# Kernel tuning notes

Hardware: AMD Instinct MI355X
Metric: run time of the kernel (lower is better)

## Reference

```python
import jax, jax.numpy as jnp
import numpy as np

NL_IN = 0.5      # init kwarg nl_in
CONS = 1e-10     # epsilon added to rates
POISSON_GAIN = 20.0

def setup_inputs() -> dict:
    key = jax.random.key(0)
    k1, k2 = jax.random.split(key)
    shape = (8, 4, 28, 256, 256)  # (bs, c, s, h, w)
    spec_data = jax.random.uniform(k1, shape, dtype=jnp.float32)
    filt = jax.random.uniform(k2, shape, dtype=jnp.float32)
    return {"spec_data": spec_data, "filter": filt}

def reference(spec_data, filter):
    # cap_data = sum over (channel, spectral) dims -> [bs, h, w], then [bs, h, w, 1]
    cap = jnp.sum(spec_data * filter, axis=(1, 2))[..., None]

    # noise synthesis (need_noise=True path)
    poisson_t = jnp.full_like(cap, POISSON_GAIN * NL_IN)
    dark_t = jnp.full_like(cap, 1.0 * NL_IN)
    gauss_t = jnp.full_like(cap, 1.0 * NL_IN)
    peak = cap + CONS

    key = jax.random.key(1)
    kp, kd, kg = jax.random.split(key, 3)
    pnoisy = jax.random.poisson(kp, peak).astype(cap.dtype)
    dnoisy = jax.random.poisson(kd, dark_t).astype(cap.dtype)
    gnoisy = jax.random.normal(kg, cap.shape, dtype=cap.dtype) * gauss_t

    noisy = (pnoisy + dnoisy + gnoisy) * poisson_t / 255.0
    return (noisy, peak, dark_t, gauss_t ** 2)
```

## Files before the change

kernel.cpp:

```cpp
#include <hip/hip_runtime.h>
#include <cstdint>
#include <cstddef>

#pragma clang fp contract(off)

#define N_PIX    524288
#define CSPLANES 112
#define PLANE    65536
#define DCH      48

struct TF2 { uint32_t a, b; };

__host__ __device__ constexpr uint32_t rotl32(uint32_t x, int d) {
  return (x << d) | (x >> (32 - d));
}

__host__ __device__ constexpr TF2 threefry(uint32_t k0, uint32_t k1,
                                           uint32_t c0, uint32_t c1) {
  uint32_t ks2 = k0 ^ k1 ^ 0x1BD11BDAu;
  uint32_t x0 = c0 + k0;
  uint32_t x1 = c1 + k1;
  const int R0[4] = {13, 15, 26, 6};
  const int R1[4] = {17, 29, 16, 24};
  for (int i = 0; i < 4; ++i) { x0 += x1; x1 = rotl32(x1, R0[i]); x1 ^= x0; }
  x0 += k1;  x1 += ks2 + 1u;
  for (int i = 0; i < 4; ++i) { x0 += x1; x1 = rotl32(x1, R1[i]); x1 ^= x0; }
  x0 += ks2; x1 += k0 + 2u;
  for (int i = 0; i < 4; ++i) { x0 += x1; x1 = rotl32(x1, R0[i]); x1 ^= x0; }
  x0 += k0;  x1 += k1 + 3u;
  for (int i = 0; i < 4; ++i) { x0 += x1; x1 = rotl32(x1, R1[i]); x1 ^= x0; }
  x0 += k1;  x1 += ks2 + 4u;
  for (int i = 0; i < 4; ++i) { x0 += x1; x1 = rotl32(x1, R0[i]); x1 ^= x0; }
  x0 += ks2; x1 += k0 + 5u;
  return TF2{x0, x1};
}

struct Chains {
  uint32_t kg0, kg1;
  uint32_t rj0a[DCH], rj0b[DCH], rj1a[DCH], rj1b[DCH];
  uint32_t kda[DCH], kdb[DCH];
  uint32_t kpa[DCH], kpb[DCH];
};

__host__ __device__ constexpr Chains make_chains() {
  Chains c{};
  TF2 kp = threefry(0u, 1u, 0u, 0u);
  TF2 kd = threefry(0u, 1u, 0u, 1u);
  TF2 kg = threefry(0u, 1u, 0u, 2u);
  c.kg0 = kg.a; c.kg1 = kg.b;
  {
    uint32_t a = kp.a, b = kp.b;
    for (int i = 0; i < DCH; ++i) {
      TF2 nk = threefry(a, b, 0u, 0u);
      TF2 s0 = threefry(a, b, 0u, 1u);
      TF2 s1 = threefry(a, b, 0u, 2u);
      c.rj0a[i] = s0.a; c.rj0b[i] = s0.b;
      c.rj1a[i] = s1.a; c.rj1b[i] = s1.b;
      a = nk.a; b = nk.b;
    }
  }
  {
    uint32_t a = kd.a, b = kd.b;
    for (int i = 0; i < DCH; ++i) {
      TF2 nk = threefry(a, b, 0u, 0u);
      TF2 sk = threefry(a, b, 0u, 1u);
      c.kda[i] = sk.a; c.kdb[i] = sk.b;
      a = nk.a; b = nk.b;
    }
  }
  {
    uint32_t a = kp.a, b = kp.b;
    for (int i = 0; i < DCH; ++i) {
      TF2 nk = threefry(a, b, 0u, 0u);
      TF2 sk = threefry(a, b, 0u, 1u);
      c.kpa[i] = sk.a; c.kpb[i] = sk.b;
      a = nk.a; b = nk.b;
    }
  }
  return c;
}

__constant__ Chains G = make_chains();

__device__ inline float u01(uint32_t k0, uint32_t k1, uint32_t j) {
  TF2 r = threefry(k0, k1, 0u, j);
  uint32_t bits = r.a ^ r.b;
  return __uint_as_float((bits >> 9) | 0x3F800000u) - 1.0f;
}

__device__ inline float xla_lgamma(float x_in) {
  float z = x_in - 1.0f;
  float x = 1.0f;
  x = x + 676.520368121885098567009190444019f    / ((z + 0.0f) + 1.0f);
  x = x + (-1259.13921672240287047156078755283f) / ((z + 1.0f) + 1.0f);
  x = x + 771.3234287776530788486528258894f      / ((z + 2.0f) + 1.0f);
  x = x + (-176.61502916214059906584551354f)     / ((z + 3.0f) + 1.0f);
  x = x + 12.507343278686904814458936853f        / ((z + 4.0f) + 1.0f);
  x = x + (-0.13857109526572011689554707f)       / ((z + 5.0f) + 1.0f);
  x = x + 9.984369578019570859563e-6f            / ((z + 6.0f) + 1.0f);
  x = x + 1.50563273514931155834e-7f             / ((z + 7.0f) + 1.0f);
  float t = 7.5f + z;
  float log_t = 2.0149030205422647f + log1pf(z / 7.5f);
  return 0.91893853320467274178f + ((z + 0.5f) - t / log_t) * log_t + logf(x);
}

__device__ inline float xla_erfinv(float xx) {
  float w = -log1pf(-(xx * xx));
  float p;
  if (w < 5.0f) {
    float ww = w - 2.5f;
    p = 2.81022636e-08f;
    p = 3.43273939e-07f + p * ww;
    p = -3.5233877e-06f + p * ww;
    p = -4.39150654e-06f + p * ww;
    p = 0.00021858087f + p * ww;
    p = -0.00125372503f + p * ww;
    p = -0.00417768164f + p * ww;
    p = 0.246640727f + p * ww;
    p = 1.50140941f + p * ww;
  } else {
    float ww = sqrtf(w) - 3.0f;
    p = -0.000200214257f;
    p = 0.000100950558f + p * ww;
    p = 0.00134934322f + p * ww;
    p = -0.00367342844f + p * ww;
    p = 0.00573950773f + p * ww;
    p = -0.0076224613f + p * ww;
    p = 0.00943887047f + p * ww;
    p = 1.00167406f + p * ww;
    p = 2.83297682f + p * ww;
  }
  return p * xx;
}

__device__ inline float xla_normal(uint32_t j) {
  const float lo = -0.999999940395355224609375f;
  float f = u01(G.kg0, G.kg1, j);
  float u = f * (1.0f - lo) + lo;
  u = fmaxf(lo, u);
  return 1.41421356237309504880f * xla_erfinv(u);
}

__device__ inline int knuth_sample(const uint32_t* ka, const uint32_t* kb,
                                   uint32_t j, float lam) {
  const float neg = -lam;
  int k = 0;
  float lp = 0.0f;
  #pragma unroll 1
  for (int i = 0; i < DCH; ++i) {
    if (!(lp > neg)) break;
    ++k;
    float uu = u01(ka[i], kb[i], j);
    lp = lp + logf(uu);
  }
  return k - 1;
}

struct RejC { float lam, loglam, a, b, inva, vr; };

__device__ inline RejC make_rc(float lam) {
  RejC rc;
  rc.lam = lam;
  rc.loglam = logf(lam);
  rc.b = 0.931f + 2.53f * sqrtf(lam);
  rc.a = -0.059f + 0.02483f * rc.b;
  rc.inva = 1.1239f + 1.1328f / (rc.b - 3.4f);
  rc.vr = 0.9277f - 3.6224f / (rc.b - 2.0f);
  return rc;
}

__device__ inline bool rej_step(const RejC& rc, uint32_t j, int i, float* kout) {
  float u = u01(G.rj0a[i], G.rj0b[i], j) - 0.5f;
  float v = u01(G.rj1a[i], G.rj1b[i], j);
  float us = 0.5f - fabsf(u);
  float k = floorf(((2.0f * rc.a / us + rc.b) * u + rc.lam) + 0.43f);
  *kout = k;
  bool accept1 = (us >= 0.07f) && (v <= rc.vr);
  if (accept1) return true;
  bool reject = (k < 0.0f) || ((us < 0.013f) && (v > us));
  if (reject) return false;
  float s = logf(v * rc.inva / (rc.a / (us * us) + rc.b));
  float t = (-rc.lam + k * rc.loglam) - xla_lgamma(k + 1.0f);
  return s <= t;
}

__device__ inline unsigned first_accept(const RejC& rc, uint32_t j) {
  unsigned F = DCH;
  #pragma unroll 1
  for (int i = 0; i < DCH; ++i) {
    float kc;
    if (rej_step(rc, j, i, &kc)) { F = (unsigned)(i + 1); break; }
  }
  return F;
}

__device__ inline float resolve_pix(const RejC& rc, float peak, uint32_t j, int T) {
  if (peak >= 10.0f) {
    float kk = -1.0f;
    #pragma unroll 1
    for (int i = T - 1; i >= 0; --i) {
      float kc;
      if (rej_step(rc, j, i, &kc)) { kk = kc; break; }
    }
    return (float)(int)kk;
  } else if (peak <= 0.0f) {
    return 0.0f;
  } else {
    return (float)knuth_sample(G.kpa, G.kpb, j, peak);
  }
}

__global__ __launch_bounds__(256) void reduce_kernel(const float* __restrict__ spec,
                                                     const float* __restrict__ filt,
                                                     float* __restrict__ out) {
  const int tid = threadIdx.x;
  const int pixbase = blockIdx.x << 10;
  const int b_img = pixbase >> 16;
  const int hw = (pixbase & 65535) + (tid << 2);
  const size_t base = (size_t)b_img * ((size_t)CSPLANES * PLANE) + (size_t)hw;
  const float* sp = spec + base;
  const float* fp = filt + base;

  float4 acc = make_float4(0.f, 0.f, 0.f, 0.f);
  #pragma unroll 1
  for (int c = 0; c < CSPLANES; c += 8) {
    float4 ss[8], ff[8];
    #pragma unroll
    for (int i = 0; i < 8; ++i) ss[i] = *reinterpret_cast<const float4*>(sp + (size_t)(c + i) * PLANE);
    #pragma unroll
    for (int i = 0; i < 8; ++i) ff[i] = *reinterpret_cast<const float4*>(fp + (size_t)(c + i) * PLANE);
    __builtin_amdgcn_sched_group_barrier(0x020, 16, 0);
    #pragma unroll
    for (int i = 0; i < 8; ++i) {
      acc.x = acc.x + ss[i].x * ff[i].x;
      acc.y = acc.y + ss[i].y * ff[i].y;
      acc.z = acc.z + ss[i].z * ff[i].z;
      acc.w = acc.w + ss[i].w * ff[i].w;
    }
    __builtin_amdgcn_sched_group_barrier(0x002, 64, 0);
  }

  const int j = pixbase + (tid << 2);
  float4 pk = make_float4(acc.x + 1e-10f, acc.y + 1e-10f,
                          acc.z + 1e-10f, acc.w + 1e-10f);
  *reinterpret_cast<float4*>(out + N_PIX + j) = pk;
}

__global__ __launch_bounds__(256) void fmax_kernel(const float* __restrict__ out,
                                                   unsigned* __restrict__ sync) {
  const int j = (blockIdx.x << 8) + threadIdx.x;
  const float pk = out[N_PIX + j];
  const RejC rc = make_rc(pk);
  unsigned F = first_accept(rc, (uint32_t)j);

  for (int off = 32; off; off >>= 1) {
    unsigned o = (unsigned)__shfl_down((int)F, off, 64);
    F = F > o ? F : o;
  }
  __shared__ unsigned sred[4];
  if ((threadIdx.x & 63) == 0) sred[threadIdx.x >> 6] = F;
  __syncthreads();
  if (threadIdx.x == 0) {
    unsigned m = sred[0];
    #pragma unroll
    for (int i = 1; i < 4; ++i) m = m > sred[i] ? m : sred[i];
    __hip_atomic_fetch_max(&sync[0], m, __ATOMIC_RELAXED, __HIP_MEMORY_SCOPE_AGENT);
  }
}

__global__ __launch_bounds__(256) void resolve_kernel(float* __restrict__ out,
                                                      const unsigned* __restrict__ sync) {
  const int j = (blockIdx.x << 8) + threadIdx.x;
  const int T = (int)__hip_atomic_load(&sync[0], __ATOMIC_RELAXED, __HIP_MEMORY_SCOPE_AGENT);
  const float pk = out[N_PIX + j];

  const float d = (float)knuth_sample(G.kda, G.kdb, (uint32_t)j, 0.5f);
  const float g = xla_normal((uint32_t)j) * 0.5f;
  const RejC rc = make_rc(pk);
  const float pv = resolve_pix(rc, pk, (uint32_t)j, T);
  const float n = ((pv + d) + g) * 10.0f / 255.0f;

  out[j]             = n;
  out[2 * N_PIX + j] = 0.5f;
  out[3 * N_PIX + j] = 0.25f;
}

extern "C" void kernel_launch(void* const* d_in, const int* in_sizes, int n_in,
                              void* d_out, int out_size, void* d_ws, size_t ws_size,
                              hipStream_t stream) {
  (void)in_sizes; (void)n_in; (void)out_size; (void)ws_size;
  const float* spec = (const float*)d_in[0];
  const float* filt = (const float*)d_in[1];
  float* out = (float*)d_out;
  unsigned* sync = (unsigned*)d_ws;
  (void)hipMemsetAsync(d_ws, 0, 2 * sizeof(unsigned), stream);
  hipLaunchKernelGGL(reduce_kernel, dim3(512), dim3(256), 0, stream, spec, filt, out);
  hipLaunchKernelGGL(fmax_kernel, dim3(2048), dim3(256), 0, stream, out, sync);
  hipLaunchKernelGGL(resolve_kernel, dim3(2048), dim3(256), 0, stream, out, sync);
}
```

Baseline: 502.6 us.

## Stream reduction through LDS with async loads and fuse fmax pass

Rewrites the channel-spectral reduction so each wave issues direct global-to-LDS loads into a double buffer, waits on vmcnt and consumes the previous stage while the next is in flight. The separate fmax kernel is folded into the reduction, so each thread computes first-accept indices for its four pixels and atomically max-reduces them without a re-read and an extra launch. The cost is 64KB of LDS per block, which limits occupancy. Per-thread work after the reduce also grows fourfold on only 512 blocks, less parallel than the old 2048-block fmax kernel.

Result: no change. 494.3 us (-1.7%).

```diff
diff --git a/kernel.cpp b/kernel.cpp
--- a/kernel.cpp
+++ b/kernel.cpp
@@ -210,10 +210,55 @@
   }
 }
 
-__global__ __launch_bounds__(256) void reduce_kernel(const float* __restrict__ spec,
-                                                     const float* __restrict__ filt,
-                                                     float* __restrict__ out) {
+typedef float f32x4 __attribute__((ext_vector_type(4)));
+
+__device__ __forceinline__ void glds16(const float* g, float* l) {
+  __builtin_amdgcn_global_load_lds(
+      (const __attribute__((address_space(1))) void*)g,
+      (__attribute__((address_space(3))) void*)l,
+      16 , 0 , 0 );
+}
+
+#define WAITC(N)                                                          \
+  asm volatile("s_waitcnt vmcnt(" #N ")" ::: "memory");                   \
+  __builtin_amdgcn_sched_barrier(0);
+
+#define LGKM0                                                             \
+  asm volatile("s_waitcnt lgkmcnt(0)" ::: "memory");                      \
+  __builtin_amdgcn_sched_barrier(0);
+
+#define STAGE(B, CBASE)                                                   \
+  {                                                                       \
+    _Pragma("unroll")                                                     \
+    for (int s = 0; s < 4; ++s)                                           \
+      glds16(sp + (size_t)((CBASE) + s) * PLANE,                          \
+             wbase + (B) * 2048 + s * 256);                               \
+    _Pragma("unroll")                                                     \
+    for (int s = 0; s < 4; ++s)                                           \
+      glds16(fp + (size_t)((CBASE) + s) * PLANE,                          \
+             wbase + (B) * 2048 + (4 + s) * 256);                         \
+  }
+
+#define CONSUME(B)                                                        \
+  {                                                                       \
+    _Pragma("unroll")                                                     \
+    for (int s = 0; s < 4; ++s) {                                         \
+      f32x4 sv = *reinterpret_cast<f32x4*>(wbase + (B) * 2048 + s * 256 + (lane << 2));       \
+      f32x4 fv = *reinterpret_cast<f32x4*>(wbase + (B) * 2048 + (4 + s) * 256 + (lane << 2)); \
+      ax = ax + sv[0] * fv[0];                                            \
+      ay = ay + sv[1] * fv[1];                                            \
+      az = az + sv[2] * fv[2];                                            \
+      aw = aw + sv[3] * fv[3];                                            \
+    }                                                                     \
+  }
+
+__global__ __launch_bounds__(256, 2) void reduce_kernel(const float* __restrict__ spec,
+                                                        const float* __restrict__ filt,
+                                                        float* __restrict__ out,
+                                                        unsigned* __restrict__ sync) {
   const int tid = threadIdx.x;
+  const int wid = tid >> 6;
+  const int lane = tid & 63;
   const int pixbase = blockIdx.x << 10;
   const int b_img = pixbase >> 16;
   const int hw = (pixbase & 65535) + (tid << 2);
@@ -221,46 +266,56 @@
   const float* sp = spec + base;
   const float* fp = filt + base;
 
-  float4 acc = make_float4(0.f, 0.f, 0.f, 0.f);
+  __shared__ float lds[16384];
+  float* wbase = &lds[wid << 12];
+
+  float ax = 0.f, ay = 0.f, az = 0.f, aw = 0.f;
+
+  STAGE(0, 0);
+  STAGE(1, 4);
   #pragma unroll 1
-  for (int c = 0; c < CSPLANES; c += 8) {
-    float4 ss[8], ff[8];
-    #pragma unroll
-    for (int i = 0; i < 8; ++i) ss[i] = *reinterpret_cast<const float4*>(sp + (size_t)(c + i) * PLANE);
-    #pragma unroll
-    for (int i = 0; i < 8; ++i) ff[i] = *reinterpret_cast<const float4*>(fp + (size_t)(c + i) * PLANE);
-    __builtin_amdgcn_sched_group_barrier(0x020, 16, 0);
-    #pragma unroll
-    for (int i = 0; i < 8; ++i) {
-      acc.x = acc.x + ss[i].x * ff[i].x;
-      acc.y = acc.y + ss[i].y * ff[i].y;
-      acc.z = acc.z + ss[i].z * ff[i].z;
-      acc.w = acc.w + ss[i].w * ff[i].w;
-    }
-    __builtin_amdgcn_sched_group_barrier(0x002, 64, 0);
-  }
+  for (int c = 0; c < 104; c += 8) {
+    WAITC(8);
+    CONSUME(0);
+    LGKM0;
+    STAGE(0, c + 8);
+    WAITC(8);
+    CONSUME(1);
+    LGKM0;
+    STAGE(1, c + 12);
+  }
+  WAITC(8);
+  CONSUME(0);
+  WAITC(0);
+  CONSUME(1);
 
   const int j = pixbase + (tid << 2);
-  float4 pk = make_float4(acc.x + 1e-10f, acc.y + 1e-10f,
-                          acc.z + 1e-10f, acc.w + 1e-10f);
-  *reinterpret_cast<float4*>(out + N_PIX + j) = pk;
-}
-
-__global__ __launch_bounds__(256) void fmax_kernel(const float* __restrict__ out,
-                                                   unsigned* __restrict__ sync) {
-  const int j = (blockIdx.x << 8) + threadIdx.x;
-  const float pk = out[N_PIX + j];
-  const RejC rc = make_rc(pk);
-  unsigned F = first_accept(rc, (uint32_t)j);
+  const float pk0 = ax + 1e-10f;
+  const float pk1 = ay + 1e-10f;
+  const float pk2 = az + 1e-10f;
+  const float pk3 = aw + 1e-10f;
+  f32x4 pkv; pkv[0] = pk0; pkv[1] = pk1; pkv[2] = pk2; pkv[3] = pk3;
+  *reinterpret_cast<f32x4*>(out + N_PIX + j) = pkv;
+
+  const uint32_t j0 = (uint32_t)j;
+  const RejC rc0 = make_rc(pk0);
+  const RejC rc1 = make_rc(pk1);
+  const RejC rc2 = make_rc(pk2);
+  const RejC rc3 = make_rc(pk3);
+  unsigned F = first_accept(rc0, j0);
+  { unsigned f = first_accept(rc1, j0 + 1u); if (f > F) F = f; }
+  { unsigned f = first_accept(rc2, j0 + 2u); if (f > F) F = f; }
+  { unsigned f = first_accept(rc3, j0 + 3u); if (f > F) F = f; }
 
   for (int off = 32; off; off >>= 1) {
     unsigned o = (unsigned)__shfl_down((int)F, off, 64);
     F = F > o ? F : o;
   }
-  __shared__ unsigned sred[4];
-  if ((threadIdx.x & 63) == 0) sred[threadIdx.x >> 6] = F;
+  unsigned* sred = reinterpret_cast<unsigned*>(lds);
   __syncthreads();
-  if (threadIdx.x == 0) {
+  if (lane == 0) sred[wid] = F;
+  __syncthreads();
+  if (tid == 0) {
     unsigned m = sred[0];
     #pragma unroll
     for (int i = 1; i < 4; ++i) m = m > sred[i] ? m : sred[i];
@@ -294,7 +349,6 @@
   float* out = (float*)d_out;
   unsigned* sync = (unsigned*)d_ws;
   (void)hipMemsetAsync(d_ws, 0, 2 * sizeof(unsigned), stream);
-  hipLaunchKernelGGL(reduce_kernel, dim3(512), dim3(256), 0, stream, spec, filt, out);
-  hipLaunchKernelGGL(fmax_kernel, dim3(2048), dim3(256), 0, stream, out, sync);
+  hipLaunchKernelGGL(reduce_kernel, dim3(512), dim3(256), 0, stream, spec, filt, out, sync);
   hipLaunchKernelGGL(resolve_kernel, dim3(2048), dim3(256), 0, stream, out, sync);
 }
```
